# Kernel tuning notes

Measured on AMD Instinct MI355X. Metric: run time of the kernel, lower is better.

## Reference

```python
import jax, jax.numpy as jnp
import numpy as np

INF = 1e10  # finite stand-in for +inf so sqrt stays well-defined


def _edt(site):
    """Exact Euclidean distance transform: distance from each pixel to the
    nearest True pixel in `site` [H, W] (0 on site pixels).
    Separable brute-force lower envelope: O(H*W*(H+W)) min-plus reductions,
    matching scipy.ndimage.distance_transform_edt when sites are nonempty."""
    H, W = site.shape
    f = jnp.where(site, 0.0, INF)                      # [H, W] squared-dist seed
    j = jnp.arange(W, dtype=jnp.float32)
    dj2 = (j[:, None] - j[None, :]) ** 2               # [W, W]
    # 1D pass along columns: g[i, j] = min_{j'} f[i, j'] + (j - j')^2
    g = jnp.min(f[:, None, :] + dj2[None, :, :], axis=2)   # [H, W]
    i = jnp.arange(H, dtype=jnp.float32)
    di2 = (i[:, None] - i[None, :]) ** 2               # [H, H]
    # 1D pass along rows: d2[i, j] = min_{i'} g[i', j] + (i - i')^2
    d2 = jnp.min(g[None, :, :] + di2[:, :, None], axis=1)  # [H, W]
    return jnp.sqrt(d2)


def _distance_map(mask):
    """mask: float binary [H, W]. Returns D = edt(1-m) + edt(m) as in the
    torch module (zero if mask is all-zeros or all-ones)."""
    m = mask > 0.5
    n = jnp.sum(m)
    dist = _edt(m) + _edt(~m)  # dist-to-foreground + dist-to-background
    degenerate = (n == 0) | (n == m.size)
    return jnp.where(degenerate, 0.0, dist)


def reference(pred, target, boundary_weight):
    # pred: [B, C, H, W] logits; target: [B, H, W] int; boundary_weight: [B, 1, H, W]
    probs = jax.nn.softmax(pred, axis=1)
    num_classes = pred.shape[1]
    w = boundary_weight[:, 0]  # [B, H, W]
    total = jnp.float32(0.0)
    for c in range(1, num_classes):  # small fixed loop over foreground classes
        t_c = (target == c).astype(jnp.float32)        # [B, H, W]
        dist_map = jax.vmap(_distance_map)(t_c)        # [B, H, W]
        error = jnp.abs(probs[:, c] - t_c)
        total = total + jnp.mean(error * w * dist_map)
    return total / max(num_classes - 1, 1)


def setup_inputs() -> dict:
    key = jax.random.key(0)
    k1, k2, k3 = jax.random.split(key, 3)
    B, C, H, W = 8, 4, 256, 256
    pred = jax.random.normal(k1, (B, C, H, W), dtype=jnp.float32)
    target = jax.random.randint(k2, (B, H, W), 0, C, dtype=jnp.int32)
    boundary_weight = jax.random.uniform(k3, (B, 1, H, W), dtype=jnp.float32)
    return {"pred": pred, "target": target, "boundary_weight": boundary_weight}
```

## Files before the change

### kernel.cpp

```cpp
#include <hip/hip_runtime.h>
#include <math.h>

constexpr int B = 8;
constexpr int C = 4;
constexpr int H = 256;
constexpr int W = 256;
constexpr int NC = C - 1;
constexpr float EDT_INF = 1e10f;
constexpr float LOSS_SCALE = 1.0f / (float)(NC * B * H * W);
constexpr int BIGI = 1 << 20;
constexpr int TI = 2;
constexpr int WR = 4;
constexpr int NROWS = TI + 2 * WR;
constexpr int MD = 10;

__device__ __forceinline__ float exact_scan(
        const int* __restrict__ target, int b, int i, int c, bool in_c,
        int j, int lane, int wid,
        unsigned long long* tmask, int (*twl)[4], int (*twf)[4],
        int (*tpl)[4], int (*tpf)[4]) {
    const int sel = in_c ? 1 : 0;
    float best2 = EDT_INF;
    for (int d = 0; d < H; ++d) {
        if (!__syncthreads_or(d == 0 || (float)(d * d) < best2)) break;
        const int nside = (d == 0) ? 1 : 2;
        for (int sd = 0; sd < nside; ++sd) {
            const int row = sd ? i + d : i - d;
            if ((unsigned)row >= (unsigned)H) continue;
            const int t2 = target[(b * H + row) * W + j];
            const unsigned long long bm = __ballot(t2 == c);
            if (lane == 0) {
                const unsigned long long bn = ~bm;
                tmask[wid] = bm;
                twl[0][wid] = bm ? ((wid << 6) + 63 - __clzll(bm)) : -BIGI;
                twf[0][wid] = bm ? ((wid << 6) + (int)__ffsll(bm) - 1) : BIGI;
                twl[1][wid] = bn ? ((wid << 6) + 63 - __clzll(bn)) : -BIGI;
                twf[1][wid] = bn ? ((wid << 6) + (int)__ffsll(bn) - 1) : BIGI;
            }
            __syncthreads();
            if (j < 8) {
                const int ss = j >> 2, w = j & 3;
                int a = -BIGI, f = BIGI;
                for (int w2 = 0; w2 < w; ++w2)  a = max(a, twl[ss][w2]);
                for (int w2 = w + 1; w2 < 4; ++w2) f = min(f, twf[ss][w2]);
                tpl[ss][w] = a; tpf[ss][w] = f;
            }
            __syncthreads();
            const unsigned long long bmm = tmask[wid];
            const unsigned long long bb2 = sel ? ~bmm : bmm;
            const unsigned long long below = bb2 << (63 - lane);
            int last = tpl[sel][wid];
            if (below) last = j - __clzll(below);
            const unsigned long long above = bb2 >> lane;
            int nxt = tpf[sel][wid];
            if (above) nxt = j + (int)__ffsll(above) - 1;
            const int fm2 = min(min(j - last, nxt - j), 256);
            const float g = (fm2 <= 255) ? (float)(fm2 * fm2) : EDT_INF;
            best2 = fminf(best2, g + (float)(d * d));
            __syncthreads();
        }
    }
    return best2;
}

__device__ __forceinline__ float win_fm2(unsigned int bb) {
    const unsigned int down2 = ((bb & 0xFFu) << 1) | 1u;
    const int dd = __clz((int)down2) - 22;
    const unsigned int up2 = ((bb >> 8) & 0x1FFu) | 0x200u;
    const int du = __ffs((int)up2) - 1;
    const int fm = min(dd, du);
    return (float)(fm * fm);
}

__global__ __launch_bounds__(256) void fused_kernel(
        const int* __restrict__ target,
        const float* __restrict__ pred,
        const float* __restrict__ wmap,
        float* __restrict__ out) {
    const int b  = blockIdx.x >> 7;
    const int i0 = (blockIdx.x & 127) << 1;
    const int j  = threadIdx.x;
    const int lane = j & 63, wid = j >> 6;

    __shared__ unsigned int smask[2][NROWS][MD];
    __shared__ float swave[4];
    __shared__ unsigned long long tmask[4];
    __shared__ int twl[2][4], twf[2][4], tpl[2][4], tpf[2][4];

    int t_own[TI];
    #pragma unroll
    for (int r = 0; r < NROWS; ++r) {
        const int row = i0 - WR + r;
        if (row < 0 || row >= H) continue;
        const int t = target[(b * H + row) * W + j];
        const unsigned long long p0 = __ballot(t & 1);
        const unsigned long long p1 = __ballot(t & 2);
        if (lane == 0) {
            smask[0][r][1 + 2 * wid] = (unsigned int)p0;
            smask[0][r][2 + 2 * wid] = (unsigned int)(p0 >> 32);
            smask[1][r][1 + 2 * wid] = (unsigned int)p1;
            smask[1][r][2 + 2 * wid] = (unsigned int)(p1 >> 32);
        }
        if (r >= WR && r < WR + TI) t_own[r - WR] = t;
    }

    float ex[TI][4], inv[TI], wv[TI];
    #pragma unroll
    for (int il = 0; il < TI; ++il) {
        const int i = i0 + il;
        wv[il] = wmap[(b * H + i) * W + j];
        const float* pp = pred + ((size_t)b * C * H + (size_t)i) * W + j;
        const float p0 = pp[0];
        const float p1 = pp[(size_t)H * W];
        const float p2 = pp[2 * (size_t)H * W];
        const float p3 = pp[3 * (size_t)H * W];
        const float mx = fmaxf(fmaxf(p0, p1), fmaxf(p2, p3));
        ex[il][0] = __expf(p0 - mx);
        ex[il][1] = __expf(p1 - mx);
        ex[il][2] = __expf(p2 - mx);
        ex[il][3] = __expf(p3 - mx);
        inv[il] = 1.0f / (ex[il][0] + ex[il][1] + ex[il][2] + ex[il][3]);
    }
    __syncthreads();

    const int s    = j - 8;
    const int idx0 = 1 + (s >> 5);
    const int sh   = s & 31;
    const int lo_clear = (j < 8) ? (8 - j) : 0;
    const int hi_clear = (j > 247) ? (j - 247) : 0;
    const unsigned int mask17 =
        (0x1FFFFu << lo_clear) & (0x1FFFFu >> hi_clear) & 0x1FFFFu;

    float best[TI][NC];
    #pragma unroll
    for (int il = 0; il < TI; ++il) {
        const int i = i0 + il;
        const unsigned int sel1 = (t_own[il] == 1) ? 0xFFFFFFFFu : 0u;
        const unsigned int sel2 = (t_own[il] == 2) ? 0xFFFFFFFFu : 0u;
        const unsigned int sel3 = (t_own[il] == 3) ? 0xFFFFFFFFu : 0u;
        float b1 = EDT_INF, b2 = EDT_INF, b3 = EDT_INF;
        #pragma unroll
        for (int dr = -WR; dr <= WR; ++dr) {
            const int row = i + dr;
            if ((unsigned)row >= (unsigned)H) continue;
            const int r = il + WR + dr;
            const unsigned long long m0 =
                ((unsigned long long)smask[0][r][idx0 + 1] << 32) | smask[0][r][idx0];
            const unsigned long long m1 =
                ((unsigned long long)smask[1][r][idx0 + 1] << 32) | smask[1][r][idx0];
            const unsigned int w0 = (unsigned int)(m0 >> sh);
            const unsigned int w1 = (unsigned int)(m1 >> sh);
            const unsigned int c1m = w0 & ~w1;
            const unsigned int c2m = w1 & ~w0;
            const unsigned int c3m = w0 & w1;
            const float drr = (float)(dr * dr);
            b1 = fminf(b1, win_fm2((c1m ^ sel1) & mask17) + drr);
            b2 = fminf(b2, win_fm2((c2m ^ sel2) & mask17) + drr);
            b3 = fminf(b3, win_fm2((c3m ^ sel3) & mask17) + drr);
        }
        best[il][0] = b1; best[il][1] = b2; best[il][2] = b3;
    }

    bool need = false;
    #pragma unroll
    for (int il = 0; il < TI; ++il)
        #pragma unroll
        for (int cc = 0; cc < NC; ++cc) need |= (best[il][cc] > 25.0f);
    if (__syncthreads_or(need)) {
        #pragma unroll
        for (int il = 0; il < TI; ++il)
            for (int cc = 1; cc <= NC; ++cc)
                best[il][cc - 1] = exact_scan(target, b, i0 + il, cc,
                                              t_own[il] == cc, j, lane, wid,
                                              tmask, twl, twf, tpl, tpf);
    }

    float loss_acc = 0.0f;
    #pragma unroll
    for (int il = 0; il < TI; ++il) {
        const float d1 = (best[il][0] < 1e9f) ? sqrtf(best[il][0]) : 0.0f;
        const float d2 = (best[il][1] < 1e9f) ? sqrtf(best[il][1]) : 0.0f;
        const float d3 = (best[il][2] < 1e9f) ? sqrtf(best[il][2]) : 0.0f;
        const float t1 = (t_own[il] == 1) ? 1.0f : 0.0f;
        const float t2 = (t_own[il] == 2) ? 1.0f : 0.0f;
        const float t3 = (t_own[il] == 3) ? 1.0f : 0.0f;
        const float iv = inv[il];
        loss_acc += wv[il] * (fabsf(ex[il][1] * iv - t1) * d1 +
                              fabsf(ex[il][2] * iv - t2) * d2 +
                              fabsf(ex[il][3] * iv - t3) * d3);
    }

    float v = loss_acc;
    for (int off = 32; off > 0; off >>= 1) v += __shfl_down(v, off, 64);
    if (lane == 0) swave[wid] = v;
    __syncthreads();
    if (j == 0)
        atomicAdd(out, (swave[0] + swave[1] + swave[2] + swave[3]) * LOSS_SCALE);
}

extern "C" void kernel_launch(void* const* d_in, const int* in_sizes, int n_in,
                              void* d_out, int out_size, void* d_ws, size_t ws_size,
                              hipStream_t stream) {
    const float* pred   = (const float*)d_in[0];
    const int*   target = (const int*)d_in[1];
    const float* wmap   = (const float*)d_in[2];
    float* out = (float*)d_out;

    fused_kernel<<<B * (H / TI), 256, 0, stream>>>(target, pred, wmap, out);
}
```

Baseline: 79.90 us.

## Use per-class bitmasks, narrower 11-bit window and merged symmetric row offsets

Stores one ballot mask per foreground class instead of two bit-planes, so per-class masks no longer have to be decoded with AND/NOT. Shrinks the column window from 17 to 11 bits and uses a bit-reverse plus find-first-set to get the nearest-site distance. Rows at +k and -k are OR-combined before a single distance lookup, and the minimum is accumulated in integers. The aim is fewer ALU ops in the local window pass. The tradeoff is one extra ballot and more shared memory, and the smaller window must still catch every pixel that avoids the exact fallback scan.

```diff
diff --git a/kernel.cpp b/kernel.cpp
--- a/kernel.cpp
+++ b/kernel.cpp
@@ -11,6 +11,7 @@
 constexpr int BIGI = 1 << 20;
 constexpr int TI = 2;
 constexpr int WR = 4;
+constexpr int WJ = 5;
 constexpr int NROWS = TI + 2 * WR;
 constexpr int MD = 10;
 
@@ -63,13 +64,9 @@
     return best2;
 }
 
-__device__ __forceinline__ float win_fm2(unsigned int bb) {
-    const unsigned int down2 = ((bb & 0xFFu) << 1) | 1u;
-    const int dd = __clz((int)down2) - 22;
-    const unsigned int up2 = ((bb >> 8) & 0x1FFu) | 0x200u;
-    const int du = __ffs((int)up2) - 1;
-    const int fm = min(dd, du);
-    return (float)(fm * fm);
+__device__ __forceinline__ unsigned win_d(unsigned u) {
+    const unsigned f = (u >> 5) | __brev(u << 26) | 0x40u;
+    return (unsigned)(__ffs((int)f) - 1);
 }
 
 __global__ __launch_bounds__(256) void fused_kernel(
@@ -82,7 +79,7 @@
     const int j  = threadIdx.x;
     const int lane = j & 63, wid = j >> 6;
 
-    __shared__ unsigned int smask[2][NROWS][MD];
+    __shared__ unsigned int smask[NC][NROWS][MD];
     __shared__ float swave[4];
     __shared__ unsigned long long tmask[4];
     __shared__ int twl[2][4], twf[2][4], tpl[2][4], tpf[2][4];
@@ -93,13 +90,16 @@
         const int row = i0 - WR + r;
         if (row < 0 || row >= H) continue;
         const int t = target[(b * H + row) * W + j];
-        const unsigned long long p0 = __ballot(t & 1);
-        const unsigned long long p1 = __ballot(t & 2);
+        const unsigned long long p1 = __ballot(t == 1);
+        const unsigned long long p2 = __ballot(t == 2);
+        const unsigned long long p3 = __ballot(t == 3);
         if (lane == 0) {
-            smask[0][r][1 + 2 * wid] = (unsigned int)p0;
-            smask[0][r][2 + 2 * wid] = (unsigned int)(p0 >> 32);
-            smask[1][r][1 + 2 * wid] = (unsigned int)p1;
-            smask[1][r][2 + 2 * wid] = (unsigned int)(p1 >> 32);
+            smask[0][r][1 + 2 * wid] = (unsigned int)p1;
+            smask[0][r][2 + 2 * wid] = (unsigned int)(p1 >> 32);
+            smask[1][r][1 + 2 * wid] = (unsigned int)p2;
+            smask[1][r][2 + 2 * wid] = (unsigned int)(p2 >> 32);
+            smask[2][r][1 + 2 * wid] = (unsigned int)p3;
+            smask[2][r][2 + 2 * wid] = (unsigned int)(p3 >> 32);
         }
         if (r >= WR && r < WR + TI) t_own[r - WR] = t;
     }
@@ -123,49 +123,49 @@
     }
     __syncthreads();
 
-    const int s    = j - 8;
+    const int s    = j - WJ;
     const int idx0 = 1 + (s >> 5);
     const int sh   = s & 31;
-    const int lo_clear = (j < 8) ? (8 - j) : 0;
-    const int hi_clear = (j > 247) ? (j - 247) : 0;
-    const unsigned int mask17 =
-        (0x1FFFFu << lo_clear) & (0x1FFFFu >> hi_clear) & 0x1FFFFu;
-
+    const int lo_clear = (j < WJ) ? (WJ - j) : 0;
+    const int hi_clear = (j > (W - 1 - WJ)) ? (j - (W - 1 - WJ)) : 0;
+    const unsigned int mask11 =
+        ((0x7FFu << lo_clear) & (0x7FFu >> hi_clear)) & 0x7FFu;
+
+    int ibest[TI][NC];
+    #pragma unroll
+    for (int c = 0; c < NC; ++c) {
+        unsigned pw[NROWS];
+        #pragma unroll
+        for (int r = 0; r < NROWS; ++r) {
+            const unsigned int* rp = &smask[c][r][0];
+            pw[r] = __builtin_amdgcn_alignbit(rp[idx0 + 1], rp[idx0], (unsigned)sh);
+        }
+        #pragma unroll
+        for (int il = 0; il < TI; ++il) {
+            const int i = i0 + il;
+            const unsigned sel = (t_own[il] == c + 1) ? 0xFFFFFFFFu : 0u;
+            unsigned d = win_d((pw[il + WR] ^ sel) & mask11);
+            int best = (int)__umul24(d, d);
+            #pragma unroll
+            for (int k = 1; k <= WR; ++k) {
+                const unsigned ua = (i + k < H)  ? (pw[il + WR + k] ^ sel) : 0u;
+                const unsigned ub = (i - k >= 0) ? (pw[il + WR - k] ^ sel) : 0u;
+                d = win_d((ua | ub) & mask11);
+                best = min(best, (int)__umul24(d, d) + k * k);
+            }
+            ibest[il][c] = best;
+        }
+    }
+
+    bool need = false;
     float best[TI][NC];
     #pragma unroll
-    for (int il = 0; il < TI; ++il) {
-        const int i = i0 + il;
-        const unsigned int sel1 = (t_own[il] == 1) ? 0xFFFFFFFFu : 0u;
-        const unsigned int sel2 = (t_own[il] == 2) ? 0xFFFFFFFFu : 0u;
-        const unsigned int sel3 = (t_own[il] == 3) ? 0xFFFFFFFFu : 0u;
-        float b1 = EDT_INF, b2 = EDT_INF, b3 = EDT_INF;
-        #pragma unroll
-        for (int dr = -WR; dr <= WR; ++dr) {
-            const int row = i + dr;
-            if ((unsigned)row >= (unsigned)H) continue;
-            const int r = il + WR + dr;
-            const unsigned long long m0 =
-                ((unsigned long long)smask[0][r][idx0 + 1] << 32) | smask[0][r][idx0];
-            const unsigned long long m1 =
-                ((unsigned long long)smask[1][r][idx0 + 1] << 32) | smask[1][r][idx0];
-            const unsigned int w0 = (unsigned int)(m0 >> sh);
-            const unsigned int w1 = (unsigned int)(m1 >> sh);
-            const unsigned int c1m = w0 & ~w1;
-            const unsigned int c2m = w1 & ~w0;
-            const unsigned int c3m = w0 & w1;
-            const float drr = (float)(dr * dr);
-            b1 = fminf(b1, win_fm2((c1m ^ sel1) & mask17) + drr);
-            b2 = fminf(b2, win_fm2((c2m ^ sel2) & mask17) + drr);
-            b3 = fminf(b3, win_fm2((c3m ^ sel3) & mask17) + drr);
-        }
-        best[il][0] = b1; best[il][1] = b2; best[il][2] = b3;
-    }
-
-    bool need = false;
-    #pragma unroll
     for (int il = 0; il < TI; ++il)
         #pragma unroll
-        for (int cc = 0; cc < NC; ++cc) need |= (best[il][cc] > 25.0f);
+        for (int cc = 0; cc < NC; ++cc) {
+            need |= (ibest[il][cc] > 25);
+            best[il][cc] = (float)ibest[il][cc];
+        }
     if (__syncthreads_or(need)) {
         #pragma unroll
         for (int il = 0; il < TI; ++il)
```

After: 80.60 us. No clear change (+0.9%).
